# Kernel optimization log

Measured on AMD Instinct MI355X. Metric: run time of the kernel, lower is better.

The kernel has to match this reference:

```python
import jax, jax.numpy as jnp
import numpy as np
from jax.scipy.linalg import cho_solve

N = 4096        # num nodes
D = 256         # in_dim == out_dim
NUM_HOPS = 2
R = 32          # subspace_dim
ETA = 0.5
EPS_SUB = 0.5   # eps in coeff = r / (n * eps^2)
LN_EPS = 1e-5


def setup_inputs() -> dict:
    rng = np.random.default_rng(0)
    K = NUM_HOPS + 1
    # sparse-ish binary adjacency mask with self loops
    mask = (rng.random((N, N)) < 0.002).astype(np.float32)
    mask = np.maximum(mask, np.eye(N, dtype=np.float32))
    deg = mask.sum(axis=1, keepdims=True)
    A = (mask / deg).astype(np.float32)          # row-stochastic propagation
    L = (np.eye(N, dtype=np.float32) - A)        # normalized Laplacian
    H = rng.standard_normal((N, D)).astype(np.float32)
    # orthonormal subspace bases per hop, as in __init__ (QR of randn)
    U = np.stack([np.linalg.qr(rng.standard_normal((D, R)))[0][:, :R] for _ in range(K)]).astype(np.float32)
    lambda_laps = np.full((K,), 0.1, dtype=np.float32)
    hop_weights = np.full((K,), 1.0 / K, dtype=np.float32)
    threshold = np.full((D,), 0.05, dtype=np.float32)
    gamma = np.ones((D,), dtype=np.float32)
    beta = np.zeros((D,), dtype=np.float32)
    return {
        "H": jnp.asarray(H), "A": jnp.asarray(A), "adj_mask": jnp.asarray(mask),
        "L": jnp.asarray(L), "U": jnp.asarray(U),
        "lambda_laps": jnp.asarray(lambda_laps), "hop_weights": jnp.asarray(hop_weights),
        "threshold": jnp.asarray(threshold), "gamma": jnp.asarray(gamma), "beta": jnp.asarray(beta),
    }


def reference(H, A, adj_mask, L, U, lambda_laps, hop_weights, threshold, gamma, beta):
    n, d = H.shape
    r = U.shape[-1]
    # multi-hop propagation
    hops = [H]
    Hk = H
    for _ in range(NUM_HOPS):
        Hk = A @ Hk
        hops.append(Hk)
    w = jax.nn.softmax(hop_weights)
    laps = jax.nn.softplus(lambda_laps)
    coeff = r / (n * EPS_SUB ** 2)
    neg = (1.0 - adj_mask) * -1e9
    I_r = jnp.eye(r, dtype=H.dtype)
    agg = jnp.zeros_like(H)        # accumulates grad_k.T, shape [n, d]
    lap_total = jnp.zeros_like(H)
    for k, H_k in enumerate(hops):
        Uk = U[k]                  # [d, r]
        Zk = Uk.T @ H_k.T          # [r, n]
        M = I_r + coeff * (Zk @ Zk.T)              # [r, r], SPD
        Lc = jnp.linalg.cholesky(M)
        M_inv = cho_solve((Lc, True), I_r)         # cholesky_inverse
        MZ = M_inv @ Zk                            # [r, n]
        scores = Zk.T @ MZ + neg                   # [n, n] masked subspace attention
        alpha = jax.nn.softmax(scores, axis=1)
        grad_k = (Uk @ (MZ @ alpha.T)).T           # [n, d]
        agg = agg + w[k] * grad_k
        lap_total = lap_total + laps[k] * (L @ H_k)
    H_half = H + ETA * agg - ETA * lap_total
    # soft-threshold (proj is None since in_dim == out_dim)
    H_out = jnp.sign(H_half) * jax.nn.relu(jnp.abs(H_half) - threshold[None, :])
    H_out = H_out + H              # residual
    mu = H_out.mean(axis=-1, keepdims=True)
    var = H_out.var(axis=-1, keepdims=True)
    H_out = (H_out - mu) / jnp.sqrt(var + LN_EPS) * gamma + beta
    # orthogonality loss over all (k, l) pairs
    K = U.shape[0]
    orth_loss = jnp.asarray(0.0, dtype=H.dtype)
    for k in range(K):
        for l in range(k, K):
            G = U[k].T @ U[l]
            orth_loss = orth_loss + jnp.sum(((G - I_r) if l == k else G) ** 2)
    lap_smooth = jnp.sum(H_out * (L @ H_out))  # trace(H^T L H)
    return H_out, orth_loss, lap_smooth, jax.lax.stop_gradient(w)
```

## Files before the change

### kernel.cpp

```cpp
#include <hip/hip_runtime.h>
#include <math.h>

#define NN 4096
#define DD 256
#define KK 3
#define RR 32
#define MAXNNZ 128

static constexpr float ETA    = 0.5f;
static constexpr float COEFF  = 0.03125f;
static constexpr float LN_EPSF = 1e-5f;

#define OFF_H1   0
#define OFF_H2   (NN*DD)
#define OFF_H3   (2*NN*DD)
#define OFF_W    OFF_H3
#define OFF_Y    (3*NN*DD)
#define OFF_P    (OFF_Y + KK*NN*RR)
#define OFF_M    (OFF_P + KK*NN*RR)
#define OFF_MINV (OFF_M + KK*RR*RR)
#define OFF_SCAL (OFF_MINV + KK*RR*RR)
#define OFF_NNZ  (OFF_SCAL + 8)
#define OFF_COLS (OFF_NNZ + NN)
#define OFF_VALS (OFF_COLS + NN*MAXNNZ)
#define OFF_PART (OFF_VALS + NN*MAXNNZ)
#define OFF_ORTH (OFF_PART + NN/4)

__global__ void k_csr_prep(const float* __restrict__ A, int* __restrict__ nnz,
                           int* __restrict__ cols, float* __restrict__ vals,
                           const float* __restrict__ hw, const float* __restrict__ ll,
                           const float* __restrict__ U,
                           float* __restrict__ ws, float* __restrict__ out) {
  int b = blockIdx.x;
  int t = threadIdx.x;
  if (b >= NN) {
    int p = b - NN;
    if (p == 6) {
      if (t == 0) {
        float m = fmaxf(fmaxf(hw[0], hw[1]), hw[2]);
        float e0 = expf(hw[0]-m), e1 = expf(hw[1]-m), e2 = expf(hw[2]-m);
        float s = e0 + e1 + e2;
        float w0 = e0/s, w1 = e1/s, w2 = e2/s;
        ws[OFF_SCAL+0] = w0; ws[OFF_SCAL+1] = w1; ws[OFF_SCAL+2] = w2;
        for (int k = 0; k < KK; ++k) {
          float x = ll[k];
          ws[OFF_SCAL+3+k] = (x > 20.f) ? x : log1pf(expf(x));
        }
        out[NN*DD + 2] = w0; out[NN*DD + 3] = w1; out[NN*DD + 4] = w2;
      }
      for (int idx = t; idx < KK*RR*RR; idx += 256) {
        int rr2 = idx % (RR*RR);
        ws[OFF_M + idx] = ((rr2 / RR) == (rr2 % RR)) ? 1.f : 0.f;
      }
      return;
    }
    int k = (p < 3) ? 0 : ((p < 5) ? 1 : 2);
    int l = (p < 3) ? p : ((p < 5) ? p - 2 : 2);
    int a0 = t >> 5, bb = t & 31;
    float s0 = 0.f, s1 = 0.f, s2 = 0.f, s3 = 0.f;
    for (int dd = 0; dd < DD; ++dd) {
      float ul = U[(size_t)l*DD*RR + dd*RR + bb];
      const float* uk = U + (size_t)k*DD*RR + dd*RR;
      s0 += uk[a0]      * ul;
      s1 += uk[a0 + 8]  * ul;
      s2 += uk[a0 + 16] * ul;
      s3 += uk[a0 + 24] * ul;
    }
    if (k == l && bb == a0)      s0 -= 1.f;
    if (k == l && bb == a0 + 8)  s1 -= 1.f;
    if (k == l && bb == a0 + 16) s2 -= 1.f;
    if (k == l && bb == a0 + 24) s3 -= 1.f;
    float sq = s0*s0 + s1*s1 + s2*s2 + s3*s3;
    #pragma unroll
    for (int o = 32; o > 0; o >>= 1) sq += __shfl_xor(sq, o, 64);
    __shared__ float red[4];
    if ((t & 63) == 0) red[t >> 6] = sq;
    __syncthreads();
    if (t == 0) ws[OFF_ORTH + p] = red[0] + red[1] + red[2] + red[3];
    return;
  }
  int i = b;
  __shared__ int cnt;
  if (t == 0) cnt = 0;
  __syncthreads();
  const float4* row4 = (const float4*)(A + (size_t)i * NN);
  for (int j0 = 0; j0 < NN/4; j0 += 256) {
    float4 v = row4[j0 + t];
    int jb = (j0 + t) * 4;
    if (v.x != 0.f) { int p = atomicAdd(&cnt,1); if (p<MAXNNZ){cols[i*MAXNNZ+p]=jb+0; vals[i*MAXNNZ+p]=v.x;} }
    if (v.y != 0.f) { int p = atomicAdd(&cnt,1); if (p<MAXNNZ){cols[i*MAXNNZ+p]=jb+1; vals[i*MAXNNZ+p]=v.y;} }
    if (v.z != 0.f) { int p = atomicAdd(&cnt,1); if (p<MAXNNZ){cols[i*MAXNNZ+p]=jb+2; vals[i*MAXNNZ+p]=v.z;} }
    if (v.w != 0.f) { int p = atomicAdd(&cnt,1); if (p<MAXNNZ){cols[i*MAXNNZ+p]=jb+3; vals[i*MAXNNZ+p]=v.w;} }
  }
  __syncthreads();
  int n = cnt < MAXNNZ ? cnt : MAXNNZ;
  int npad = (n + 7) & ~7;
  for (int e = n + t; e < npad; e += 256) {
    cols[i*MAXNNZ + e] = i;
    vals[i*MAXNNZ + e] = 0.f;
  }
  if (t == 0) nnz[i] = n;
}

__global__ void k_spmvy(const float* __restrict__ X, float* __restrict__ Hout,
                        const int* __restrict__ nnz, const int* __restrict__ cols,
                        const float* __restrict__ vals,
                        const float* __restrict__ Uo, float* __restrict__ Yo,
                        const float* __restrict__ Un, float* __restrict__ Yn) {
  int t = threadIdx.x;
  int r = t >> 6, lane = t & 63;
  int row = blockIdx.x * 4 + r;
  int d4 = lane * 4;
  int n = nnz[row];
  int npad = (n + 7) & ~7;
  const int* ci = cols + row*MAXNNZ;
  const float* vi = vals + row*MAXNNZ;
  float4 acc = {0.f, 0.f, 0.f, 0.f};
  float4 own = {0.f, 0.f, 0.f, 0.f};
  for (int e0 = 0; e0 < npad; e0 += 8) {
    int4 c0 = *(const int4*)(ci + e0);
    int4 c1 = *(const int4*)(ci + e0 + 4);
    float4 v0 = *(const float4*)(vi + e0);
    float4 v1 = *(const float4*)(vi + e0 + 4);
    float4 x0 = *(const float4*)(X + (size_t)c0.x*DD + d4);
    float4 x1 = *(const float4*)(X + (size_t)c0.y*DD + d4);
    float4 x2 = *(const float4*)(X + (size_t)c0.z*DD + d4);
    float4 x3 = *(const float4*)(X + (size_t)c0.w*DD + d4);
    float4 x4 = *(const float4*)(X + (size_t)c1.x*DD + d4);
    float4 x5 = *(const float4*)(X + (size_t)c1.y*DD + d4);
    float4 x6 = *(const float4*)(X + (size_t)c1.z*DD + d4);
    float4 x7 = *(const float4*)(X + (size_t)c1.w*DD + d4);
    if (c0.x == row) own = x0;
    if (c0.y == row) own = x1;
    if (c0.z == row) own = x2;
    if (c0.w == row) own = x3;
    if (c1.x == row) own = x4;
    if (c1.y == row) own = x5;
    if (c1.z == row) own = x6;
    if (c1.w == row) own = x7;
    acc.x += v0.x*x0.x + v0.y*x1.x + v0.z*x2.x + v0.w*x3.x + v1.x*x4.x + v1.y*x5.x + v1.z*x6.x + v1.w*x7.x;
    acc.y += v0.x*x0.y + v0.y*x1.y + v0.z*x2.y + v0.w*x3.y + v1.x*x4.y + v1.y*x5.y + v1.z*x6.y + v1.w*x7.y;
    acc.z += v0.x*x0.z + v0.y*x1.z + v0.z*x2.z + v0.w*x3.z + v1.x*x4.z + v1.y*x5.z + v1.z*x6.z + v1.w*x7.z;
    acc.w += v0.x*x0.w + v0.y*x1.w + v0.z*x2.w + v0.w*x3.w + v1.x*x4.w + v1.y*x5.w + v1.z*x6.w + v1.w*x7.w;
  }
  *(float4*)(Hout + (size_t)row*DD + d4) = acc;
  if (!Uo && !Un) return;
  __shared__ float Hs[4][2][DD];
  *(float4*)&Hs[r][0][d4] = own;
  *(float4*)&Hs[r][1][d4] = acc;
  __syncthreads();
  int c = lane & 31, h = lane >> 5;
  if (Uo) {
    float part = 0.f;
    #pragma unroll 8
    for (int d = h*128; d < h*128 + 128; ++d) part += Hs[r][0][d] * Uo[d*RR + c];
    part += __shfl_xor(part, 32, 64);
    if (h == 0) Yo[(size_t)row*RR + c] = part;
  }
  if (Un) {
    float part = 0.f;
    #pragma unroll 8
    for (int d = h*128; d < h*128 + 128; ++d) part += Hs[r][1][d] * Un[d*RR + c];
    part += __shfl_xor(part, 32, 64);
    if (h == 0) Yn[(size_t)row*RR + c] = part;
  }
}

__global__ __launch_bounds__(1024) void k_gram(const float* __restrict__ Y, float* __restrict__ M) {
  int k = blockIdx.y;
  __shared__ float Ys[128*RR];
  int t = threadIdx.x;
  const float* Yk = Y + (size_t)k*NN*RR + (size_t)blockIdx.x*128*RR;
  for (int idx = t; idx < 128*RR; idx += 1024) Ys[idx] = Yk[idx];
  __syncthreads();
  int a = t >> 5, b = t & 31;
  float s = 0.f;
  for (int i = 0; i < 128; ++i) s += Ys[i*RR + a] * Ys[i*RR + b];
  atomicAdd(&M[k*RR*RR + a*RR + b], COEFF * s);
}

__global__ __launch_bounds__(256) void k_gj(const float* __restrict__ M, float* __restrict__ Minv,
                                            const float* __restrict__ U, float* __restrict__ W) {
  int k = blockIdx.x;
  __shared__ float B[RR][2*RR];
  int t = threadIdx.x;
  for (int idx = t; idx < RR*2*RR; idx += 256) {
    int r = idx >> 6, c = idx & 63;
    B[r][c] = (c < RR) ? M[k*RR*RR + r*RR + c] : ((c - RR == r) ? 1.f : 0.f);
  }
  __syncthreads();
  int c = t & 63, r0 = t >> 6;
  for (int j = 0; j < RR; ++j) {
    float bjc = B[j][c];
    float pinv = 1.f / B[j][j];
    float f[8];
    #pragma unroll
    for (int q = 0; q < 8; ++q) f[q] = B[r0 + 4*q][j];
    __syncthreads();
    float pb = pinv * bjc;
    #pragma unroll
    for (int q = 0; q < 8; ++q) {
      int r = r0 + 4*q;
      B[r][c] = (r == j) ? pb : (B[r][c] - f[q] * pb);
    }
    __syncthreads();
  }
  for (int idx = t; idx < RR*RR; idx += 256)
    Minv[k*RR*RR + (idx >> 5)*RR + (idx & 31)] = B[idx >> 5][RR + (idx & 31)];
  for (int idx = t; idx < DD*RR; idx += 256) {
    int d = idx >> 5, rr2 = idx & 31;
    const float* ud = U + (size_t)k*DD*RR + (size_t)d*RR;
    float s = 0.f;
    #pragma unroll 8
    for (int a = 0; a < RR; ++a) s += ud[a] * B[a][RR + rr2];
    W[(size_t)k*DD*RR + idx] = s;
  }
}

__global__ __launch_bounds__(256) void k_attn(const float* __restrict__ Y, const float* __restrict__ Minv,
                       float* __restrict__ P, const int* __restrict__ nnz,
                       const int* __restrict__ cols) {
  int k = blockIdx.y;
  int t = threadIdx.x;
  int w = t >> 6, lane = t & 63;
  int i = blockIdx.x * 4 + w;
  const float* Yk = Y + (size_t)k*NN*RR;
  __shared__ float Mi[RR*RR];
  __shared__ float Yi[4][RR];
  __shared__ float qv[4][RR];
  __shared__ float sc[4][MAXNNZ];
  for (int idx = t; idx < RR*RR; idx += 256) Mi[idx] = Minv[k*RR*RR + idx];
  if (lane < RR) Yi[w][lane] = Yk[(size_t)i*RR + lane];
  sc[w][lane] = -1e30f; sc[w][lane+64] = -1e30f;
  __syncthreads();
  if (lane < RR) {
    float s = 0.f;
    #pragma unroll 8
    for (int a = 0; a < RR; ++a) s += Mi[a*RR + lane] * Yi[w][a];
    qv[w][lane] = s;
  }
  __syncthreads();
  int n = nnz[i], npad = (n + 7) & ~7;
  const int* ci = cols + i*MAXNNZ;
  for (int e = lane; e < npad; e += 64) {
    const float4* yr = (const float4*)(Yk + (size_t)ci[e]*RR);
    float s = 0.f;
    #pragma unroll
    for (int qq = 0; qq < 8; ++qq) {
      float4 yv = yr[qq];
      s += yv.x*qv[w][4*qq] + yv.y*qv[w][4*qq+1] + yv.z*qv[w][4*qq+2] + yv.w*qv[w][4*qq+3];
    }
    sc[w][e] = (e < n) ? s : -1e30f;
  }
  __syncthreads();
  float s0 = sc[w][lane], s1 = sc[w][lane+64];
  float m = fmaxf(s0, s1);
  #pragma unroll
  for (int o = 32; o > 0; o >>= 1) m = fmaxf(m, __shfl_xor(m, o, 64));
  float e0v = expf(s0 - m), e1v = expf(s1 - m);
  sc[w][lane] = e0v; sc[w][lane+64] = e1v;
  float l = e0v + e1v;
  #pragma unroll
  for (int o = 32; o > 0; o >>= 1) l += __shfl_xor(l, o, 64);
  float linv = 1.f / l;
  __syncthreads();
  int c = lane & 31, h = lane >> 5;
  float acc = 0.f;
  for (int e = h; e < npad; e += 2) acc += sc[w][e] * Yk[(size_t)ci[e]*RR + c];
  acc += __shfl_xor(acc, 32, 64);
  if (lane < RR) P[(size_t)k*NN*RR + (size_t)i*RR + lane] = acc * linv;
}

__global__ void k_epi(const float* __restrict__ H0, const float* __restrict__ ws,
                      const float* __restrict__ thr,
                      const float* __restrict__ gma, const float* __restrict__ bta,
                      const int* __restrict__ nnz, const int* __restrict__ cols,
                      const float* __restrict__ vals,
                      float* __restrict__ out) {
  __shared__ float Us[DD][RR+1];
  __shared__ float Ps[8][KK*RR];
  int t = threadIdx.x;
  int ty = t >> 5, tx = t & 31;
  int row0 = blockIdx.x * 8;
  int i = row0 + ty;
  const float* P    = ws + OFF_P;
  const float* scal = ws + OFF_SCAL;
  const float* W    = ws + OFF_W;
  const float* H1   = ws + OFF_H1;
  const float* H2   = ws + OFF_H2;
  float h3a[8];
  #pragma unroll
  for (int j = 0; j < 8; ++j) h3a[j] = 0.f;
  {
    int n = nnz[i], npad = (n + 7) & ~7;
    const int* ci = cols + (size_t)i*MAXNNZ;
    const float* vi = vals + (size_t)i*MAXNNZ;
    for (int e = 0; e < npad; e += 2) {
      int ca = ci[e], cb = ci[e+1];
      float va = vi[e], vb = vi[e+1];
      const float* ra = H2 + (size_t)ca*DD + tx;
      const float* rb = H2 + (size_t)cb*DD + tx;
      #pragma unroll
      for (int j = 0; j < 8; ++j) h3a[j] += va * ra[32*j] + vb * rb[32*j];
    }
  }
  for (int idx = t; idx < 8*KK*RR; idx += 256) {
    int rl = idx / (KK*RR), kr = idx % (KK*RR);
    int k = kr / RR, rr2 = kr % RR;
    Ps[rl][kr] = P[(size_t)k*NN*RR + (size_t)(row0+rl)*RR + rr2];
  }
  float lp0 = scal[3], lp1 = scal[4], lp2 = scal[5];
  float gacc[8];
  #pragma unroll
  for (int j = 0; j < 8; ++j) gacc[j] = 0.f;
  for (int k = 0; k < KK; ++k) {
    __syncthreads();
    for (int idx = t; idx < DD*RR; idx += 256) Us[idx >> 5][idx & 31] = W[(size_t)k*DD*RR + idx];
    __syncthreads();
    float wk = scal[k];
    #pragma unroll
    for (int j = 0; j < 8; ++j) {
      int d = tx + 32*j;
      float s = 0.f;
      #pragma unroll
      for (int rr2 = 0; rr2 < RR; ++rr2) s += Ps[ty][k*RR + rr2] * Us[d][rr2];
      gacc[j] += wk * s;
    }
  }
  float v[8]; float sum = 0.f, sumsq = 0.f;
  #pragma unroll
  for (int j = 0; j < 8; ++j) {
    int d = tx + 32*j;
    size_t idx = (size_t)i*DD + d;
    float h0 = H0[idx], h1 = H1[idx], h2 = H2[idx];
    float lap = lp0*(h0-h1) + lp1*(h1-h2) + lp2*(h2-h3a[j]);
    float hf = h0 + ETA*gacc[j] - ETA*lap;
    float a = fabsf(hf) - thr[d];
    float sft = (a > 0.f) ? copysignf(a, hf) : 0.f;
    float x = sft + h0;
    v[j] = x; sum += x; sumsq += x*x;
  }
  #pragma unroll
  for (int o = 16; o > 0; o >>= 1) {
    sum   += __shfl_xor(sum, o, 32);
    sumsq += __shfl_xor(sumsq, o, 32);
  }
  float mu  = sum * (1.f/DD);
  float var = sumsq * (1.f/DD) - mu*mu;
  float inv = rsqrtf(var + LN_EPSF);
  #pragma unroll
  for (int j = 0; j < 8; ++j) {
    int d = tx + 32*j;
    out[(size_t)i*DD + d] = (v[j] - mu) * inv * gma[d] + bta[d];
  }
}

__global__ void k_lapsm(const float* __restrict__ Hout, const int* __restrict__ nnz,
                        const int* __restrict__ cols, const float* __restrict__ vals,
                        float* __restrict__ partial) {
  int t = threadIdx.x;
  int row = blockIdx.x * 4 + (t >> 6);
  int d4 = (t & 63) * 4;
  int n = nnz[row];
  int npad = (n + 7) & ~7;
  const int* ci = cols + row*MAXNNZ;
  const float* vi = vals + row*MAXNNZ;
  float4 acc = {0.f, 0.f, 0.f, 0.f};
  for (int e0 = 0; e0 < npad; e0 += 8) {
    int4 c0 = *(const int4*)(ci + e0);
    int4 c1 = *(const int4*)(ci + e0 + 4);
    float4 v0 = *(const float4*)(vi + e0);
    float4 v1 = *(const float4*)(vi + e0 + 4);
    float4 x0 = *(const float4*)(Hout + (size_t)c0.x*DD + d4);
    float4 x1 = *(const float4*)(Hout + (size_t)c0.y*DD + d4);
    float4 x2 = *(const float4*)(Hout + (size_t)c0.z*DD + d4);
    float4 x3 = *(const float4*)(Hout + (size_t)c0.w*DD + d4);
    float4 x4 = *(const float4*)(Hout + (size_t)c1.x*DD + d4);
    float4 x5 = *(const float4*)(Hout + (size_t)c1.y*DD + d4);
    float4 x6 = *(const float4*)(Hout + (size_t)c1.z*DD + d4);
    float4 x7 = *(const float4*)(Hout + (size_t)c1.w*DD + d4);
    acc.x += v0.x*x0.x + v0.y*x1.x + v0.z*x2.x + v0.w*x3.x + v1.x*x4.x + v1.y*x5.x + v1.z*x6.x + v1.w*x7.x;
    acc.y += v0.x*x0.y + v0.y*x1.y + v0.z*x2.y + v0.w*x3.y + v1.x*x4.y + v1.y*x5.y + v1.z*x6.y + v1.w*x7.y;
    acc.z += v0.x*x0.z + v0.y*x1.z + v0.z*x2.z + v0.w*x3.z + v1.x*x4.z + v1.y*x5.z + v1.z*x6.z + v1.w*x7.z;
    acc.w += v0.x*x0.w + v0.y*x1.w + v0.z*x2.w + v0.w*x3.w + v1.x*x4.w + v1.y*x5.w + v1.z*x6.w + v1.w*x7.w;
  }
  float4 h = *(const float4*)(Hout + (size_t)row*DD + d4);
  float part = h.x*(h.x-acc.x) + h.y*(h.y-acc.y) + h.z*(h.z-acc.z) + h.w*(h.w-acc.w);
  #pragma unroll
  for (int o = 32; o > 0; o >>= 1) part += __shfl_xor(part, o, 64);
  __shared__ float red[4];
  if ((t & 63) == 0) red[t >> 6] = part;
  __syncthreads();
  if (t == 0) partial[blockIdx.x] = red[0] + red[1] + red[2] + red[3];
}

__global__ void k_red(const float* __restrict__ ws, float* __restrict__ out) {
  const float* partial = ws + OFF_PART;
  int t = threadIdx.x;
  float4 p = *(const float4*)(partial + t*4);
  float s = p.x + p.y + p.z + p.w;
  #pragma unroll
  for (int o = 32; o > 0; o >>= 1) s += __shfl_xor(s, o, 64);
  __shared__ float red[4];
  if ((t & 63) == 0) red[t >> 6] = s;
  __syncthreads();
  if (t == 0) {
    out[1] = red[0] + red[1] + red[2] + red[3];
    const float* op = ws + OFF_ORTH;
    out[0] = op[0] + op[1] + op[2] + op[3] + op[4] + op[5];
  }
}

extern "C" void kernel_launch(void* const* d_in, const int* in_sizes, int n_in,
                              void* d_out, int out_size, void* d_ws, size_t ws_size,
                              hipStream_t stream) {
  const float* H   = (const float*)d_in[0];
  const float* A   = (const float*)d_in[1];
  const float* U   = (const float*)d_in[4];
  const float* ll  = (const float*)d_in[5];
  const float* hw  = (const float*)d_in[6];
  const float* thr = (const float*)d_in[7];
  const float* gma = (const float*)d_in[8];
  const float* bta = (const float*)d_in[9];
  float* out = (float*)d_out;
  float* ws  = (float*)d_ws;
  int* nnz   = (int*)(ws + OFF_NNZ);
  int* cols  = (int*)(ws + OFF_COLS);
  float* vals = ws + OFF_VALS;
  float* Y = ws + OFF_Y;

  k_csr_prep<<<NN + 7, 256, 0, stream>>>(A, nnz, cols, vals, hw, ll, U, ws, out);
  k_spmvy<<<NN/4, 256, 0, stream>>>(H, ws + OFF_H1, nnz, cols, vals,
                                    U, Y, U + (size_t)DD*RR, Y + (size_t)NN*RR);
  k_spmvy<<<NN/4, 256, 0, stream>>>(ws + OFF_H1, ws + OFF_H2, nnz, cols, vals,
                                    nullptr, nullptr, U + (size_t)2*DD*RR, Y + (size_t)2*NN*RR);
  dim3 g32(NN/128, KK);
  k_gram<<<g32, 1024, 0, stream>>>(Y, ws + OFF_M);
  k_gj<<<KK, 256, 0, stream>>>(ws + OFF_M, ws + OFF_MINV, U, ws + OFF_W);
  dim3 gattn(NN/4, KK);
  k_attn<<<gattn, 256, 0, stream>>>(Y, ws + OFF_MINV, ws + OFF_P, nnz, cols);
  k_epi<<<NN/8, 256, 0, stream>>>(H, ws, thr, gma, bta, nnz, cols, vals, out);
  k_lapsm<<<NN/4, 256, 0, stream>>>(out, nnz, cols, vals, ws + OFF_PART);
  k_red<<<1, 256, 0, stream>>>(ws, out + NN*DD);
}
```

Measured before the change: 313.6 us.

## Move third-hop SpMM into separate kernel and parallelize attention score dot products

```diff
diff --git a/kernel.cpp b/kernel.cpp
--- a/kernel.cpp
+++ b/kernel.cpp
@@ -14,7 +14,6 @@
 #define OFF_H1   0
 #define OFF_H2   (NN*DD)
 #define OFF_H3   (2*NN*DD)
-#define OFF_W    OFF_H3
 #define OFF_Y    (3*NN*DD)
 #define OFF_P    (OFF_Y + KK*NN*RR)
 #define OFF_M    (OFF_P + KK*NN*RR)
@@ -25,6 +24,7 @@
 #define OFF_VALS (OFF_COLS + NN*MAXNNZ)
 #define OFF_PART (OFF_VALS + NN*MAXNNZ)
 #define OFF_ORTH (OFF_PART + NN/4)
+#define OFF_W    (OFF_ORTH + 8)
 
 __global__ void k_csr_prep(const float* __restrict__ A, int* __restrict__ nnz,
                            int* __restrict__ cols, float* __restrict__ vals,
@@ -239,20 +239,24 @@
     for (int a = 0; a < RR; ++a) s += Mi[a*RR + lane] * Yi[w][a];
     qv[w][lane] = s;
   }
-  __syncthreads();
+  int g = lane >> 2, a4 = lane & 3;
+  const float* qq = &qv[w][8*a4];
+  float q0 = qq[0], q1 = qq[1], q2 = qq[2], q3 = qq[3];
+  float q4 = qq[4], q5 = qq[5], q6 = qq[6], q7 = qq[7];
   int n = nnz[i], npad = (n + 7) & ~7;
   const int* ci = cols + i*MAXNNZ;
-  for (int e = lane; e < npad; e += 64) {
-    const float4* yr = (const float4*)(Yk + (size_t)ci[e]*RR);
-    float s = 0.f;
-    #pragma unroll
-    for (int qq = 0; qq < 8; ++qq) {
-      float4 yv = yr[qq];
-      s += yv.x*qv[w][4*qq] + yv.y*qv[w][4*qq+1] + yv.z*qv[w][4*qq+2] + yv.w*qv[w][4*qq+3];
-    }
-    sc[w][e] = (e < n) ? s : -1e30f;
-  }
-  __syncthreads();
+  for (int e0 = 0; e0 < npad; e0 += 16) {
+    int e = e0 + g;
+    int ee = (e < npad) ? e : 0;
+    int col = ci[ee];
+    const float4* yr = (const float4*)(Yk + (size_t)col*RR + 8*a4);
+    float4 y0 = yr[0], y1 = yr[1];
+    float s = y0.x*q0 + y0.y*q1 + y0.z*q2 + y0.w*q3
+            + y1.x*q4 + y1.y*q5 + y1.z*q6 + y1.w*q7;
+    s += __shfl_xor(s, 1, 64);
+    s += __shfl_xor(s, 2, 64);
+    if (a4 == 0 && e < npad) sc[w][e] = (e < n) ? s : -1e30f;
+  }
   float s0 = sc[w][lane], s1 = sc[w][lane+64];
   float m = fmaxf(s0, s1);
   #pragma unroll
@@ -263,7 +267,6 @@
   #pragma unroll
   for (int o = 32; o > 0; o >>= 1) l += __shfl_xor(l, o, 64);
   float linv = 1.f / l;
-  __syncthreads();
   int c = lane & 31, h = lane >> 5;
   float acc = 0.f;
   for (int e = h; e < npad; e += 2) acc += sc[w][e] * Yk[(size_t)ci[e]*RR + c];
@@ -274,36 +277,15 @@
 __global__ void k_epi(const float* __restrict__ H0, const float* __restrict__ ws,
                       const float* __restrict__ thr,
                       const float* __restrict__ gma, const float* __restrict__ bta,
-                      const int* __restrict__ nnz, const int* __restrict__ cols,
-                      const float* __restrict__ vals,
                       float* __restrict__ out) {
   __shared__ float Us[DD][RR+1];
   __shared__ float Ps[8][KK*RR];
   int t = threadIdx.x;
   int ty = t >> 5, tx = t & 31;
   int row0 = blockIdx.x * 8;
-  int i = row0 + ty;
   const float* P    = ws + OFF_P;
   const float* scal = ws + OFF_SCAL;
   const float* W    = ws + OFF_W;
-  const float* H1   = ws + OFF_H1;
-  const float* H2   = ws + OFF_H2;
-  float h3a[8];
-  #pragma unroll
-  for (int j = 0; j < 8; ++j) h3a[j] = 0.f;
-  {
-    int n = nnz[i], npad = (n + 7) & ~7;
-    const int* ci = cols + (size_t)i*MAXNNZ;
-    const float* vi = vals + (size_t)i*MAXNNZ;
-    for (int e = 0; e < npad; e += 2) {
-      int ca = ci[e], cb = ci[e+1];
-      float va = vi[e], vb = vi[e+1];
-      const float* ra = H2 + (size_t)ca*DD + tx;
-      const float* rb = H2 + (size_t)cb*DD + tx;
-      #pragma unroll
-      for (int j = 0; j < 8; ++j) h3a[j] += va * ra[32*j] + vb * rb[32*j];
-    }
-  }
   for (int idx = t; idx < 8*KK*RR; idx += 256) {
     int rl = idx / (KK*RR), kr = idx % (KK*RR);
     int k = kr / RR, rr2 = kr % RR;
@@ -327,13 +309,17 @@
       gacc[j] += wk * s;
     }
   }
+  int i = row0 + ty;
+  const float* H1 = ws + OFF_H1;
+  const float* H2 = ws + OFF_H2;
+  const float* H3 = ws + OFF_H3;
   float v[8]; float sum = 0.f, sumsq = 0.f;
   #pragma unroll
   for (int j = 0; j < 8; ++j) {
     int d = tx + 32*j;
     size_t idx = (size_t)i*DD + d;
-    float h0 = H0[idx], h1 = H1[idx], h2 = H2[idx];
-    float lap = lp0*(h0-h1) + lp1*(h1-h2) + lp2*(h2-h3a[j]);
+    float h0 = H0[idx], h1 = H1[idx], h2 = H2[idx], h3 = H3[idx];
+    float lap = lp0*(h0-h1) + lp1*(h1-h2) + lp2*(h2-h3);
     float hf = h0 + ETA*gacc[j] - ETA*lap;
     float a = fabsf(hf) - thr[d];
     float sft = (a > 0.f) ? copysignf(a, hf) : 0.f;
@@ -434,12 +420,14 @@
                                     U, Y, U + (size_t)DD*RR, Y + (size_t)NN*RR);
   k_spmvy<<<NN/4, 256, 0, stream>>>(ws + OFF_H1, ws + OFF_H2, nnz, cols, vals,
                                     nullptr, nullptr, U + (size_t)2*DD*RR, Y + (size_t)2*NN*RR);
+  k_spmvy<<<NN/4, 256, 0, stream>>>(ws + OFF_H2, ws + OFF_H3, nnz, cols, vals,
+                                    nullptr, nullptr, nullptr, nullptr);
   dim3 g32(NN/128, KK);
   k_gram<<<g32, 1024, 0, stream>>>(Y, ws + OFF_M);
   k_gj<<<KK, 256, 0, stream>>>(ws + OFF_M, ws + OFF_MINV, U, ws + OFF_W);
   dim3 gattn(NN/4, KK);
   k_attn<<<gattn, 256, 0, stream>>>(Y, ws + OFF_MINV, ws + OFF_P, nnz, cols);
-  k_epi<<<NN/8, 256, 0, stream>>>(H, ws, thr, gma, bta, nnz, cols, vals, out);
+  k_epi<<<NN/8, 256, 0, stream>>>(H, ws, thr, gma, bta, out);
   k_lapsm<<<NN/4, 256, 0, stream>>>(out, nnz, cols, vals, ws + OFF_PART);
   k_red<<<1, 256, 0, stream>>>(ws, out + NN*DD);
 }
```

Result: no change. 307.7 us (-1.9%).
